# Kernel optimization log

Hardware: AMD Instinct MI355X
Metric: run time of the kernel (lower is better)

## Reference

```python
import jax, jax.numpy as jnp
import numpy as np

N_HEADS = 16


def setup_inputs() -> dict:
    key = jax.random.key(0)
    ks = jax.random.split(key, 4)
    B, S, E = 4, 2048, 1024
    x = jax.random.normal(ks[0], (B, S, E), dtype=jnp.float32)
    w_attn = jax.random.normal(ks[1], (E, 3 * E), dtype=jnp.float32) * 0.02
    b_attn = jnp.zeros((3 * E,), dtype=jnp.float32)
    w_proj = jax.random.normal(ks[2], (E, E), dtype=jnp.float32) * 0.02
    b_proj = jnp.zeros((E,), dtype=jnp.float32)
    return {"x": x, "w_attn": w_attn, "b_attn": b_attn, "w_proj": w_proj, "b_proj": b_proj}


def reference(x, w_attn, b_attn, w_proj, b_proj):
    B, S, E = x.shape
    H = N_HEADS
    D = E // H
    # fused QKV projection (Conv1D: x @ W + b)
    qkv = x @ w_attn + b_attn                     # [B, S, 3E]
    q, k, v = jnp.split(qkv, 3, axis=-1)          # each [B, S, E]
    q = q.reshape(B, S, H, D).transpose(0, 2, 1, 3)  # [B, H, S, D]
    k = k.reshape(B, S, H, D).transpose(0, 2, 1, 3)
    v = v.reshape(B, S, H, D).transpose(0, 2, 1, 3)
    # scaled QK^T
    scores = jnp.einsum('bhqd,bhkd->bhqk', q, k) / jnp.sqrt(jnp.asarray(D, dtype=x.dtype))
    # causal mask via where with dtype-min fill (matches torch.where(c_m, w, finfo.min))
    causal = jnp.tril(jnp.ones((S, S), dtype=bool))  # [S, S]
    scores = jnp.where(causal[None, None, :, :], scores, jnp.finfo(scores.dtype).min)
    attn = jax.nn.softmax(scores, axis=-1)        # [B, H, S, S]
    o = jnp.einsum('bhqk,bhkd->bhqd', attn, v)    # [B, H, S, D]
    o = o.transpose(0, 2, 1, 3).reshape(B, S, E)  # merge heads
    return o @ w_proj + b_proj                    # output projection
```

## Files before the change

kernel.cpp:

```cpp
#include <hip/hip_runtime.h>
#include <stdint.h>


typedef __bf16 bf16;
typedef __bf16 bf16x4 __attribute__((ext_vector_type(4)));
typedef __bf16 bf16x8 __attribute__((ext_vector_type(8)));
typedef float  f32x4  __attribute__((ext_vector_type(4)));

#define DEV __device__ __forceinline__

DEV void async_copy16(bf16* lds, const bf16* g) {
  __builtin_amdgcn_global_load_lds(
      (__attribute__((address_space(1))) void*)(uintptr_t)g,
      (__attribute__((address_space(3))) void*)(uint32_t)(uintptr_t)lds,
      16, 0, 0);
}

__global__ __launch_bounds__(256) void cast_x_kernel(const float* __restrict__ in,
                                                     bf16* __restrict__ out, int n4) {
  int i = blockIdx.x * blockDim.x + threadIdx.x;
  int stride = gridDim.x * blockDim.x;
  for (; i < n4; i += stride) {
    float4 v = ((const float4*)in)[i];
    bf16x4 o = { (bf16)v.x, (bf16)v.y, (bf16)v.z, (bf16)v.w };
    *(bf16x4*)(out + (size_t)i * 4) = o;
  }
}

__global__ __launch_bounds__(256) void transpose_cast_kernel(const float* __restrict__ W,
                                                             bf16* __restrict__ Wt,
                                                             int Kd, int Nd) {
  __shared__ alignas(16) bf16 T[64 * 80];
  const int t = threadIdx.x;
  const int n0 = blockIdx.x * 64;
  const int k0 = blockIdx.y * 64;
#pragma unroll
  for (int i = 0; i < 4; ++i) {
    int idx = t + i * 256;
    int r  = idx >> 4;
    int c4 = (idx & 15) * 4;
    float4 v = *(const float4*)(W + (size_t)(k0 + r) * Nd + n0 + c4);
    bf16x4 o = { (bf16)v.x, (bf16)v.y, (bf16)v.z, (bf16)v.w };
    *(bf16x4*)(&T[r * 80 + c4]) = o;
  }
  __syncthreads();
#pragma unroll
  for (int i = 0; i < 2; ++i) {
    int idx = t + i * 256;
    int n = idx >> 3;
    int c = idx & 7;
    bf16x8 o;
#pragma unroll
    for (int j = 0; j < 8; ++j) o[j] = T[(c * 8 + j) * 80 + n];
    *(bf16x8*)(Wt + (size_t)(n0 + n) * Kd + k0 + c * 8) = o;
  }
}

__global__ __launch_bounds__(256) void vtrans_kernel(const bf16* __restrict__ qkv,
                                                     bf16* __restrict__ vt) {
  __shared__ alignas(16) bf16 T[64 * 80];
  const int t  = threadIdx.x;
  const int s0 = blockIdx.x * 64;
  const int bh = blockIdx.y;
  const int b = bh >> 4, h = bh & 15;
#pragma unroll
  for (int i = 0; i < 2; ++i) {
    int idx = t + i * 256;
    int s = idx >> 3, c = idx & 7;
    bf16x8 v = *(const bf16x8*)(qkv + (size_t)(b * 2048 + s0 + s) * 3072 + 2048 + h * 64 + c * 8);
    *(bf16x8*)(&T[s * 80 + c * 8]) = v;
  }
  __syncthreads();
#pragma unroll
  for (int i = 0; i < 2; ++i) {
    int idx = t + i * 256;
    int d = idx >> 3, c = idx & 7;
    bf16x8 o;
#pragma unroll
    for (int j = 0; j < 8; ++j) {
      int pos = c * 8 + j;
      int key = (pos & 32) | (((pos >> 2) & 1) << 4) | (((pos >> 3) & 3) << 2) | (pos & 3);
      o[j] = T[key * 80 + d];
    }
    *(bf16x8*)(vt + (size_t)(bh * 64 + d) * 2048 + s0 + c * 8) = o;
  }
}

template <typename OutT>
__global__ __launch_bounds__(512, 4) void gemm256_kernel(const bf16* __restrict__ A,
                                                         const bf16* __restrict__ Bt,
                                                         const float* __restrict__ bias,
                                                         OutT* __restrict__ C,
                                                         int M, int N, int K,
                                                         float qscale, int qcols,
                                                         int nbx) {
  __shared__ alignas(16) bf16 As[3][256 * 32];
  __shared__ alignas(16) bf16 Bs[3][128 * 32];

  const int tid  = threadIdx.x;
  const int lane = tid & 63;
  const int w    = tid >> 6;
  const int wm = w >> 1, wn = w & 1;
  const int l15 = lane & 15, l16 = lane >> 4;

  const int nwg = (int)gridDim.x;
  const int cpx = nwg >> 3;
  const int swz = ((int)blockIdx.x & 7) * cpx + ((int)blockIdx.x >> 3);
  const int m0 = (swz / nbx) * 256;
  const int n0 = (swz % nbx) * 128;

  const int c0  = w * 64 + lane;
  const int rA0 = c0 >> 2, sA0 = c0 & 3;
  const int rA1 = rA0 + 128;
  const bf16* srcA0 = A  + (size_t)(m0 + rA0) * K + 8 * (sA0 ^ ((rA0 >> 1) & 3));
  const bf16* srcA1 = A  + (size_t)(m0 + rA1) * K + 8 * (sA0 ^ ((rA1 >> 1) & 3));
  const bf16* srcB  = Bt + (size_t)(n0 + rA0) * K + 8 * (sA0 ^ ((rA0 >> 1) & 3));

#define STAGE_TILE(buf, kt)                                       \
  {                                                               \
    const int k0_ = (kt) * 32;                                    \
    async_copy16(&As[buf][(w * 64) * 8],         srcA0 + k0_);    \
    async_copy16(&As[buf][(512 + w * 64) * 8],   srcA1 + k0_);    \
    async_copy16(&Bs[buf][(w * 64) * 8],         srcB  + k0_);    \
  }

  f32x4 acc[4][4];
  f32x4 zf = {0.f, 0.f, 0.f, 0.f};
#pragma unroll
  for (int i = 0; i < 4; ++i)
#pragma unroll
    for (int j = 0; j < 4; ++j) acc[i][j] = zf;

  const int KT = K >> 5;
  STAGE_TILE(0, 0)
  STAGE_TILE(1, 1)

  const int soff = 8 * (l16 ^ ((l15 >> 1) & 3));

  int bufc = 0;
  int bufs = 2;
  for (int kt = 0; kt < KT; ++kt) {
    if (kt < KT - 1) { asm volatile("s_waitcnt vmcnt(3)" ::: "memory"); }
    else             { asm volatile("s_waitcnt vmcnt(0)" ::: "memory"); }
    __builtin_amdgcn_s_barrier();
    asm volatile("" ::: "memory");
    if (kt + 2 < KT) STAGE_TILE(bufs, kt + 2)

    bf16x8 bfr[4], afr[4];
#pragma unroll
    for (int n = 0; n < 4; ++n) {
      int rb = wn * 64 + n * 16 + l15;
      bfr[n] = *(const bf16x8*)(&Bs[bufc][rb * 32 + soff]);
    }
#pragma unroll
    for (int m = 0; m < 4; ++m) {
      int ra = wm * 64 + m * 16 + l15;
      afr[m] = *(const bf16x8*)(&As[bufc][ra * 32 + soff]);
    }
    __builtin_amdgcn_s_setprio(1);
#pragma unroll
    for (int m = 0; m < 4; ++m)
#pragma unroll
      for (int n = 0; n < 4; ++n)
        acc[m][n] = __builtin_amdgcn_mfma_f32_16x16x32_bf16(afr[m], bfr[n], acc[m][n], 0, 0, 0);
    __builtin_amdgcn_s_setprio(0);
    asm volatile("" ::: "memory");
    bufc = (bufc == 2) ? 0 : bufc + 1;
    bufs = (bufs == 2) ? 0 : bufs + 1;
  }

#pragma unroll
  for (int n = 0; n < 4; ++n) {
    int col = n0 + wn * 64 + n * 16 + l15;
    float bb = bias[col];
    float sc2 = (col < qcols) ? qscale : 1.0f;
#pragma unroll
    for (int m = 0; m < 4; ++m) {
#pragma unroll
      for (int reg = 0; reg < 4; ++reg) {
        int row = m0 + wm * 64 + m * 16 + l16 * 4 + reg;
        C[(size_t)row * N + col] = (OutT)((acc[m][n][reg] + bb) * sc2);
      }
    }
  }
#undef STAGE_TILE
}

__global__ __launch_bounds__(256, 4) void flash_kernel(const bf16* __restrict__ qkv,
                                                       const bf16* __restrict__ vt,
                                                       bf16* __restrict__ obuf) {
  constexpr int S = 2048, E3 = 3072;
  __shared__ alignas(16) bf16 Ks[2][64 * 64];
  __shared__ alignas(16) bf16 Vs[2][64 * 64];

  const int tid  = threadIdx.x;
  const int lane = tid & 63;
  const int w    = tid >> 6;
  const int bx = blockIdx.x;
  const int bh = blockIdx.y;
  const int b = bh >> 4, h = bh & 15;
  const int l15 = lane & 15, l16 = lane >> 4;

  const int sr  = lane >> 3;
  const int scc = lane & 7;
  const int r0 = w * 16 + sr;
  const int r1 = w * 16 + 8 + sr;
  const bf16* kst0 = qkv + (size_t)(b * S + r0) * E3 + 1024 + h * 64 + 8 * (scc ^ sr);
  const bf16* kst1 = qkv + (size_t)(b * S + r1) * E3 + 1024 + h * 64 + 8 * (scc ^ sr);
  const bf16* vst0 = vt + (size_t)(bh * 64 + r0) * S + 8 * (scc ^ sr);
  const bf16* vst1 = vt + (size_t)(bh * 64 + r1) * S + 8 * (scc ^ sr);

  const int xsw = l15 & 7;
  const uint32_t rdA = (uint32_t)(l15 * 128 + 16 * (l16 ^ xsw));
  const uint32_t rdB = (uint32_t)(l15 * 128 + 16 * ((4 + l16) ^ xsw));

#define KV_STAGE(buf, kv0_)                                          \
  {                                                                  \
    async_copy16(Ks[buf] + (w * 2) * 512,     kst0 + (size_t)(kv0_) * E3); \
    async_copy16(Ks[buf] + (w * 2 + 1) * 512, kst1 + (size_t)(kv0_) * E3); \
    async_copy16(Vs[buf] + (w * 2) * 512,     vst0 + (kv0_));        \
    async_copy16(Vs[buf] + (w * 2 + 1) * 512, vst1 + (kv0_));        \
  }

  for (int half = 0; half < 2; ++half) {
    const int t = half ? (15 - bx) : bx;
    const int q0 = t * 128;
    const int wq0 = q0 + w * 32;
    const int nsteps = 2 * t + 2;

    KV_STAGE(0, 0)

    bf16x8 qf[2][2];
    {
      const bf16* qbase = qkv + (size_t)(b * S + wq0) * E3 + h * 64;
#pragma unroll
      for (int s = 0; s < 2; ++s)
#pragma unroll
        for (int dk = 0; dk < 2; ++dk)
          qf[s][dk] = *(const bf16x8*)(qbase + (size_t)(s * 16 + l15) * E3 + (dk * 4 + l16) * 8);
    }

    float lstate[2] = {0.f, 0.f};
    f32x4 oacc[2][4];
    f32x4 zf = {0.f, 0.f, 0.f, 0.f};
#pragma unroll
    for (int s = 0; s < 2; ++s)
#pragma unroll
      for (int i = 0; i < 4; ++i) oacc[s][i] = zf;

    __syncthreads();

#define FLASH_STEP(CUR, STEPIDX)                                                  \
    {                                                                             \
      const int kv0 = (STEPIDX) * 64;                                             \
      if ((STEPIDX) + 1 < nsteps) KV_STAGE((CUR) ^ 1, kv0 + 64)                   \
      if (kv0 <= wq0 + 31) {                     \
        f32x4 sv[2][4];                                                           \
        _Pragma("unroll")                                                         \
        for (int kf = 0; kf < 4; ++kf) { sv[0][kf] = zf; sv[1][kf] = zf; }        \
        __builtin_amdgcn_s_setprio(1);                                            \
        _Pragma("unroll")                                                         \
        for (int kf = 0; kf < 4; ++kf) {                                          \
          bf16x8 k0 = *(const bf16x8*)((const char*)Ks[CUR] + rdA + kf * 2048);   \
          sv[0][kf] = __builtin_amdgcn_mfma_f32_16x16x32_bf16(k0, qf[0][0], sv[0][kf], 0, 0, 0); \
          sv[1][kf] = __builtin_amdgcn_mfma_f32_16x16x32_bf16(k0, qf[1][0], sv[1][kf], 0, 0, 0); \
          bf16x8 k1 = *(const bf16x8*)((const char*)Ks[CUR] + rdB + kf * 2048);   \
          sv[0][kf] = __builtin_amdgcn_mfma_f32_16x16x32_bf16(k1, qf[0][1], sv[0][kf], 0, 0, 0); \
          sv[1][kf] = __builtin_amdgcn_mfma_f32_16x16x32_bf16(k1, qf[1][1], sv[1][kf], 0, 0, 0); \
        }                                                                         \
        __builtin_amdgcn_s_setprio(0);                                            \
        bf16x8 pb[2][2];                                                          \
        _Pragma("unroll")                                                         \
        for (int s = 0; s < 2; ++s) {                                             \
          if (kv0 + 63 > wq0 + s * 16) {                \
            const int qrow_ = wq0 + s * 16 + l15;                                 \
            _Pragma("unroll")                                                     \
            for (int kf = 0; kf < 4; ++kf)                                        \
              _Pragma("unroll")                                                   \
              for (int reg = 0; reg < 4; ++reg) {                                 \
                int key = kv0 + kf * 16 + l16 * 4 + reg;                          \
                if (key > qrow_) sv[s][kf][reg] = -1e30f;                         \
              }                                                                   \
          }                                                                       \
          float rsum = 0.f;                                                       \
          _Pragma("unroll")                                                       \
          for (int kf = 0; kf < 4; ++kf)                                          \
            _Pragma("unroll")                                                     \
            for (int reg = 0; reg < 4; ++reg) {                                   \
              float p = __builtin_amdgcn_exp2f(sv[s][kf][reg]);                   \
              sv[s][kf][reg] = p;                                                 \
              rsum += p;                                                          \
            }                                                                     \
          rsum += __shfl_xor(rsum, 16);                                           \
          rsum += __shfl_xor(rsum, 32);                                           \
          lstate[s] += rsum;                                                      \
          _Pragma("unroll")                                                       \
          for (int kc = 0; kc < 2; ++kc) {                                        \
            bf16x8 tq;                                                            \
            tq[0] = (bf16)sv[s][2 * kc][0];  tq[1] = (bf16)sv[s][2 * kc][1];      \
            tq[2] = (bf16)sv[s][2 * kc][2];  tq[3] = (bf16)sv[s][2 * kc][3];      \
            tq[4] = (bf16)sv[s][2 * kc + 1][0]; tq[5] = (bf16)sv[s][2 * kc + 1][1]; \
            tq[6] = (bf16)sv[s][2 * kc + 1][2]; tq[7] = (bf16)sv[s][2 * kc + 1][3]; \
            pb[s][kc] = tq;                                                       \
          }                                                                       \
        }                                                                         \
        __builtin_amdgcn_s_setprio(1);                                            \
        _Pragma("unroll")                                                         \
        for (int nf = 0; nf < 4; ++nf) {                                          \
          bf16x8 vf0 = *(const bf16x8*)((const char*)Vs[CUR] + rdA + nf * 2048);  \
          oacc[0][nf] = __builtin_amdgcn_mfma_f32_16x16x32_bf16(vf0, pb[0][0], oacc[0][nf], 0, 0, 0); \
          oacc[1][nf] = __builtin_amdgcn_mfma_f32_16x16x32_bf16(vf0, pb[1][0], oacc[1][nf], 0, 0, 0); \
          bf16x8 vf1 = *(const bf16x8*)((const char*)Vs[CUR] + rdB + nf * 2048);  \
          oacc[0][nf] = __builtin_amdgcn_mfma_f32_16x16x32_bf16(vf1, pb[0][1], oacc[0][nf], 0, 0, 0); \
          oacc[1][nf] = __builtin_amdgcn_mfma_f32_16x16x32_bf16(vf1, pb[1][1], oacc[1][nf], 0, 0, 0); \
        }                                                                         \
        __builtin_amdgcn_s_setprio(0);                                            \
      }                                                                           \
      __syncthreads();          \
    }

    for (int step = 0; step < nsteps; step += 2) {
      FLASH_STEP(0, step)
      FLASH_STEP(1, step + 1)
    }
#undef FLASH_STEP

#pragma unroll
    for (int s = 0; s < 2; ++s) {
      float inv = 1.0f / lstate[s];
      int qrow = wq0 + s * 16 + l15;
#pragma unroll
      for (int nf = 0; nf < 4; ++nf) {
        bf16x4 o4 = { (bf16)(oacc[s][nf][0] * inv), (bf16)(oacc[s][nf][1] * inv),
                      (bf16)(oacc[s][nf][2] * inv), (bf16)(oacc[s][nf][3] * inv) };
        *(bf16x4*)(obuf + (size_t)(b * S + qrow) * 1024 + h * 64 + nf * 16 + l16 * 4) = o4;
      }
    }
  }
#undef KV_STAGE
}

extern "C" void kernel_launch(void* const* d_in, const int* in_sizes, int n_in,
                              void* d_out, int out_size, void* d_ws, size_t ws_size,
                              hipStream_t stream) {
  (void)in_sizes; (void)n_in; (void)out_size; (void)ws_size;
  const float* x      = (const float*)d_in[0];
  const float* w_attn = (const float*)d_in[1];
  const float* b_attn = (const float*)d_in[2];
  const float* w_proj = (const float*)d_in[3];
  const float* b_proj = (const float*)d_in[4];
  float* out = (float*)d_out;

  char* ws = (char*)d_ws;
  bf16* xb  = (bf16*)(ws + 0);
  bf16* wat = (bf16*)(ws + 16777216);
  bf16* wpt = (bf16*)(ws + 23068672);
  bf16* qkv = (bf16*)(ws + 25165824);
  bf16* vt  = (bf16*)(ws + 75497472);
  bf16* ob  = (bf16*)(ws + 92274688);

  const float QSCALE = 0.18033688011112042f;

  cast_x_kernel<<<2048, 256, 0, stream>>>(x, xb, 8192 * 1024 / 4);
  transpose_cast_kernel<<<dim3(48, 16), 256, 0, stream>>>(w_attn, wat, 1024, 3072);
  transpose_cast_kernel<<<dim3(16, 16), 256, 0, stream>>>(w_proj, wpt, 1024, 1024);
  gemm256_kernel<bf16><<<768, 512, 0, stream>>>(xb, wat, b_attn, qkv,
                                                8192, 3072, 1024, QSCALE, 1024, 24);
  vtrans_kernel<<<dim3(32, 64), 256, 0, stream>>>(qkv, vt);
  flash_kernel<<<dim3(8, 64), 256, 0, stream>>>(qkv, vt, ob);
  gemm256_kernel<float><<<256, 512, 0, stream>>>(ob, wpt, b_proj, out,
                                                 8192, 1024, 1024, 1.0f, 0, 8);
}
```

Before: 164.6 us.

## Fuse V transpose into QKV GEMM epilogue and split flash tiles per block

Result: slower. 173.0 us (+5.1%).

```diff
diff --git a/kernel.cpp b/kernel.cpp
--- a/kernel.cpp
+++ b/kernel.cpp
@@ -56,41 +56,12 @@
   }
 }
 
-__global__ __launch_bounds__(256) void vtrans_kernel(const bf16* __restrict__ qkv,
-                                                     bf16* __restrict__ vt) {
-  __shared__ alignas(16) bf16 T[64 * 80];
-  const int t  = threadIdx.x;
-  const int s0 = blockIdx.x * 64;
-  const int bh = blockIdx.y;
-  const int b = bh >> 4, h = bh & 15;
-#pragma unroll
-  for (int i = 0; i < 2; ++i) {
-    int idx = t + i * 256;
-    int s = idx >> 3, c = idx & 7;
-    bf16x8 v = *(const bf16x8*)(qkv + (size_t)(b * 2048 + s0 + s) * 3072 + 2048 + h * 64 + c * 8);
-    *(bf16x8*)(&T[s * 80 + c * 8]) = v;
-  }
-  __syncthreads();
-#pragma unroll
-  for (int i = 0; i < 2; ++i) {
-    int idx = t + i * 256;
-    int d = idx >> 3, c = idx & 7;
-    bf16x8 o;
-#pragma unroll
-    for (int j = 0; j < 8; ++j) {
-      int pos = c * 8 + j;
-      int key = (pos & 32) | (((pos >> 2) & 1) << 4) | (((pos >> 3) & 3) << 2) | (pos & 3);
-      o[j] = T[key * 80 + d];
-    }
-    *(bf16x8*)(vt + (size_t)(bh * 64 + d) * 2048 + s0 + c * 8) = o;
-  }
-}
-
-template <typename OutT>
+template <typename OutT, bool FUSE_VT>
 __global__ __launch_bounds__(512, 4) void gemm256_kernel(const bf16* __restrict__ A,
                                                          const bf16* __restrict__ Bt,
                                                          const float* __restrict__ bias,
                                                          OutT* __restrict__ C,
+                                                         bf16* __restrict__ vtout,
                                                          int M, int N, int K,
                                                          float qscale, int qcols,
                                                          int nbx) {
@@ -173,13 +144,29 @@
   for (int n = 0; n < 4; ++n) {
     int col = n0 + wn * 64 + n * 16 + l15;
     float bb = bias[col];
-    float sc2 = (col < qcols) ? qscale : 1.0f;
-#pragma unroll
-    for (int m = 0; m < 4; ++m) {
-#pragma unroll
-      for (int reg = 0; reg < 4; ++reg) {
-        int row = m0 + wm * 64 + m * 16 + l16 * 4 + reg;
-        C[(size_t)row * N + col] = (OutT)((acc[m][n][reg] + bb) * sc2);
+    if (FUSE_VT && col >= 2048) {
+      int hh = (col - 2048) >> 6, d = (col - 2048) & 63;
+#pragma unroll
+      for (int m = 0; m < 4; ++m) {
+#pragma unroll
+        for (int reg = 0; reg < 4; ++reg) {
+          int row = m0 + wm * 64 + m * 16 + l16 * 4 + reg;
+          int s = row & 2047;
+          int key = s & 63;
+          int pos = (key & 32) | (((key >> 2) & 3) << 3) | (((key >> 4) & 1) << 2) | (key & 3);
+          size_t vtaddr = ((size_t)((row >> 11) * 16 + hh) * 64 + d) * 2048 + (s & ~63) + pos;
+          vtout[vtaddr] = (bf16)(acc[m][n][reg] + bb);
+        }
+      }
+    } else {
+      float sc2 = (col < qcols) ? qscale : 1.0f;
+#pragma unroll
+      for (int m = 0; m < 4; ++m) {
+#pragma unroll
+        for (int reg = 0; reg < 4; ++reg) {
+          int row = m0 + wm * 64 + m * 16 + l16 * 4 + reg;
+          C[(size_t)row * N + col] = (OutT)((acc[m][n][reg] + bb) * sc2);
+        }
       }
     }
   }
@@ -196,7 +183,7 @@
   const int tid  = threadIdx.x;
   const int lane = tid & 63;
   const int w    = tid >> 6;
-  const int bx = blockIdx.x;
+  const int t  = 15 - (int)blockIdx.x;
   const int bh = blockIdx.y;
   const int b = bh >> 4, h = bh & 15;
   const int l15 = lane & 15, l16 = lane >> 4;
@@ -222,33 +209,31 @@
     async_copy16(Vs[buf] + (w * 2 + 1) * 512, vst1 + (kv0_));        \
   }
 
-  for (int half = 0; half < 2; ++half) {
-    const int t = half ? (15 - bx) : bx;
-    const int q0 = t * 128;
-    const int wq0 = q0 + w * 32;
-    const int nsteps = 2 * t + 2;
-
-    KV_STAGE(0, 0)
-
-    bf16x8 qf[2][2];
-    {
-      const bf16* qbase = qkv + (size_t)(b * S + wq0) * E3 + h * 64;
-#pragma unroll
-      for (int s = 0; s < 2; ++s)
-#pragma unroll
-        for (int dk = 0; dk < 2; ++dk)
-          qf[s][dk] = *(const bf16x8*)(qbase + (size_t)(s * 16 + l15) * E3 + (dk * 4 + l16) * 8);
-    }
-
-    float lstate[2] = {0.f, 0.f};
-    f32x4 oacc[2][4];
-    f32x4 zf = {0.f, 0.f, 0.f, 0.f};
+  const int q0 = t * 128;
+  const int wq0 = q0 + w * 32;
+  const int nsteps = 2 * t + 2;
+
+  KV_STAGE(0, 0)
+
+  bf16x8 qf[2][2];
+  {
+    const bf16* qbase = qkv + (size_t)(b * S + wq0) * E3 + h * 64;
 #pragma unroll
     for (int s = 0; s < 2; ++s)
 #pragma unroll
-      for (int i = 0; i < 4; ++i) oacc[s][i] = zf;
-
-    __syncthreads();
+      for (int dk = 0; dk < 2; ++dk)
+        qf[s][dk] = *(const bf16x8*)(qbase + (size_t)(s * 16 + l15) * E3 + (dk * 4 + l16) * 8);
+  }
+
+  float lstate[2] = {0.f, 0.f};
+  f32x4 oacc[2][4];
+  f32x4 zf = {0.f, 0.f, 0.f, 0.f};
+#pragma unroll
+  for (int s = 0; s < 2; ++s)
+#pragma unroll
+    for (int i = 0; i < 4; ++i) oacc[s][i] = zf;
+
+  __syncthreads();
 
 #define FLASH_STEP(CUR, STEPIDX)                                                  \
     {                                                                             \
@@ -319,22 +304,21 @@
       __syncthreads();          \
     }
 
-    for (int step = 0; step < nsteps; step += 2) {
-      FLASH_STEP(0, step)
-      FLASH_STEP(1, step + 1)
-    }
+  for (int step = 0; step < nsteps; step += 2) {
+    FLASH_STEP(0, step)
+    FLASH_STEP(1, step + 1)
+  }
 #undef FLASH_STEP
 
 #pragma unroll
-    for (int s = 0; s < 2; ++s) {
-      float inv = 1.0f / lstate[s];
-      int qrow = wq0 + s * 16 + l15;
-#pragma unroll
-      for (int nf = 0; nf < 4; ++nf) {
-        bf16x4 o4 = { (bf16)(oacc[s][nf][0] * inv), (bf16)(oacc[s][nf][1] * inv),
-                      (bf16)(oacc[s][nf][2] * inv), (bf16)(oacc[s][nf][3] * inv) };
-        *(bf16x4*)(obuf + (size_t)(b * S + qrow) * 1024 + h * 64 + nf * 16 + l16 * 4) = o4;
-      }
+  for (int s = 0; s < 2; ++s) {
+    float inv = 1.0f / lstate[s];
+    int qrow = wq0 + s * 16 + l15;
+#pragma unroll
+    for (int nf = 0; nf < 4; ++nf) {
+      bf16x4 o4 = { (bf16)(oacc[s][nf][0] * inv), (bf16)(oacc[s][nf][1] * inv),
+                    (bf16)(oacc[s][nf][2] * inv), (bf16)(oacc[s][nf][3] * inv) };
+      *(bf16x4*)(obuf + (size_t)(b * S + qrow) * 1024 + h * 64 + nf * 16 + l16 * 4) = o4;
     }
   }
 #undef KV_STAGE
@@ -364,10 +348,9 @@
   cast_x_kernel<<<2048, 256, 0, stream>>>(x, xb, 8192 * 1024 / 4);
   transpose_cast_kernel<<<dim3(48, 16), 256, 0, stream>>>(w_attn, wat, 1024, 3072);
   transpose_cast_kernel<<<dim3(16, 16), 256, 0, stream>>>(w_proj, wpt, 1024, 1024);
-  gemm256_kernel<bf16><<<768, 512, 0, stream>>>(xb, wat, b_attn, qkv,
-                                                8192, 3072, 1024, QSCALE, 1024, 24);
-  vtrans_kernel<<<dim3(32, 64), 256, 0, stream>>>(qkv, vt);
-  flash_kernel<<<dim3(8, 64), 256, 0, stream>>>(qkv, vt, ob);
-  gemm256_kernel<float><<<256, 512, 0, stream>>>(ob, wpt, b_proj, out,
-                                                 8192, 1024, 1024, 1.0f, 0, 8);
-}
+  gemm256_kernel<bf16, true><<<768, 512, 0, stream>>>(xb, wat, b_attn, qkv, vt,
+                                                      8192, 3072, 1024, QSCALE, 1024, 24);
+  flash_kernel<<<dim3(16, 64), 256, 0, stream>>>(qkv, vt, ob);
+  gemm256_kernel<float, false><<<256, 512, 0, stream>>>(ob, wpt, b_proj, out, nullptr,
+                                                        8192, 1024, 1024, 1.0f, 0, 8);
+}
```
